# Optimization experiments

Measured on AMD Instinct MI355X. Metric: run time of the kernel, lower is better.

## Reference

```python
import jax, jax.numpy as jnp
import numpy as np

NUM_HEADS = 16


def setup_inputs() -> dict:
    key = jax.random.key(0)
    k1, k2, k3, k4 = jax.random.split(key, 4)
    in_dim, out_dim = 1024, 1024
    x = jax.random.normal(k1, (4, 2048, in_dim), dtype=jnp.float32)
    # nn.Linear weights stored as [out, in]; we keep that convention.
    s = 1.0 / np.sqrt(in_dim)
    Wq = jax.random.uniform(k2, (out_dim, in_dim), jnp.float32, -s, s)
    Wk = jax.random.uniform(k3, (out_dim, in_dim), jnp.float32, -s, s)
    Wv = jax.random.uniform(k4, (out_dim, in_dim), jnp.float32, -s, s)
    return {"x": x, "Wq": Wq, "Wk": Wk, "Wv": Wv}


def reference(x, Wq, Wk, Wv):
    b, n, _ = x.shape
    out_dim = Wq.shape[0]
    h = NUM_HEADS
    d = out_dim // h  # head_dim

    def split_heads(t):  # [b,n,out] -> [b,h,n,d]
        return t.reshape(b, n, h, d).transpose(0, 2, 1, 3)

    q = split_heads(x @ Wq.T)
    k = split_heads(x @ Wk.T)
    v = split_heads(x @ Wv.T)

    scores = jnp.einsum("bhqd,bhkd->bhqk", q, k) / jnp.sqrt(jnp.float32(d))
    causal = jnp.tril(jnp.ones((n, n), dtype=bool))
    scores = jnp.where(causal, scores, -jnp.inf)
    attn = jax.nn.softmax(scores, axis=-1)
    out = jnp.einsum("bhqk,bhkd->bhqd", attn, v)
    return out.transpose(0, 2, 1, 3).reshape(b, n, out_dim)
```

## Files before the change

### kernel.cpp

```cpp
#include <hip/hip_runtime.h>

typedef __attribute__((ext_vector_type(8))) short short8;
typedef __attribute__((ext_vector_type(4))) short short4v;
typedef __attribute__((ext_vector_type(4))) float floatx4;
typedef __attribute__((ext_vector_type(16))) float floatx16;
typedef __attribute__((ext_vector_type(2))) int iv2;

#define GLOBAL_AS __attribute__((address_space(1)))
#define LDS_AS __attribute__((address_space(3)))

__device__ __forceinline__ short f2bs(float f) {
    union { float f; unsigned u; } v; v.f = f;
    unsigned r = v.u + 0x7fffu + ((v.u >> 16) & 1u);
    return (short)(r >> 16);
}

#if __has_builtin(__builtin_amdgcn_cvt_pk_bf16_f32)
typedef __attribute__((ext_vector_type(2))) __bf16 bf16x2;
__device__ __forceinline__ unsigned pk2(float a, float b) {
    union { bf16x2 v; unsigned u; } u;
    u.v = __builtin_amdgcn_cvt_pk_bf16_f32(a, b);
    return u.u;
}
#else
__device__ __forceinline__ unsigned pk2(float a, float b) {
    union { float f; unsigned u; } x, y; x.f = a; y.f = b;
    return ((y.u + 0x8000u) & 0xffff0000u) | ((x.u + 0x8000u) >> 16);
}
#endif

__global__ __launch_bounds__(256) void cast_all(const float* __restrict__ x,
                                                const float* __restrict__ Wq,
                                                const float* __restrict__ Wk,
                                                const float* __restrict__ Wv,
                                                short* __restrict__ xb,
                                                short* __restrict__ wb) {
    int b = blockIdx.x;
    int t = threadIdx.x;
    const float* src;
    short* dst;
    int idx;
    if (b < 8192) {
        src = x; dst = xb; idx = b * 1024 + t * 4;
    } else {
        int r = b - 8192;
        int wz = r >> 10;
        src = (wz == 0) ? Wq : (wz == 1) ? Wk : Wv;
        dst = wb + wz * (1 << 20);
        idx = (r & 1023) * 1024 + t * 4;
    }
    float4 v = *(const float4*)(src + idx);
    short4v o;
    o.x = f2bs(v.x); o.y = f2bs(v.y); o.z = f2bs(v.z); o.w = f2bs(v.w);
    *(short4v*)(dst + idx) = o;
}

__global__ __launch_bounds__(256) void qkv_gemm(const short* __restrict__ xb,
                                                const short* __restrict__ wb,
                                                short* __restrict__ qout,
                                                short* __restrict__ kout,
                                                short* __restrict__ vtout) {
    __shared__ short As[2][128 * 64];
    __shared__ short Bs[2][128 * 64];
    const int K = 1024;
    int tid = threadIdx.x;
    int lane = tid & 63;
    int wid = tid >> 6;
    int quad = lane >> 4;
    int l16 = lane & 15;
    int wm = (wid >> 1) * 64;
    int wn = (wid & 1) * 64;
    int bx = blockIdx.x;
    int bm = ((bx >> 3) + ((bx & 7) << 3)) * 128;
    int bn = blockIdx.y * 128;
    const short* W = wb + (size_t)blockIdx.z * K * 1024;

    floatx4 acc[4][4];
#pragma unroll
    for (int i = 0; i < 4; i++)
#pragma unroll
        for (int j = 0; j < 4; j++) acc[i][j] = (floatx4){0.f, 0.f, 0.f, 0.f};

    int srow = tid >> 3;
    int ssw = ((tid & 7) ^ (srow & 7)) * 8;

#define STAGE_AB(cb, kk) do { \
    _Pragma("unroll") for (int l = 0; l < 4; l++) { \
        const short* g = xb + (size_t)(bm + srow + l * 32) * K + (kk) + ssw; \
        __builtin_amdgcn_global_load_lds((const GLOBAL_AS void*)g, \
            (LDS_AS void*)(&As[cb][0] + tid * 8 + l * 2048), 16, 0, 0); \
    } \
    _Pragma("unroll") for (int l = 0; l < 4; l++) { \
        const short* g = W + (size_t)(bn + srow + l * 32) * K + (kk) + ssw; \
        __builtin_amdgcn_global_load_lds((const GLOBAL_AS void*)g, \
            (LDS_AS void*)(&Bs[cb][0] + tid * 8 + l * 2048), 16, 0, 0); \
    } \
} while (0)

    STAGE_AB(0, 0);

    for (int T = 0; T < 16; T++) {
        int cur = T & 1;
        __builtin_amdgcn_sched_barrier(0);
        __builtin_amdgcn_s_barrier();
        __builtin_amdgcn_sched_barrier(0);
        if (T < 15) {
            STAGE_AB(cur ^ 1, (T + 1) * 64);
            asm volatile("s_waitcnt vmcnt(8)" ::: "memory");
        } else {
            asm volatile("s_waitcnt vmcnt(0)" ::: "memory");
        }
        __builtin_amdgcn_sched_barrier(0);
        __builtin_amdgcn_s_barrier();
        __builtin_amdgcn_sched_barrier(0);

        const short* Ac = &As[cur][0];
        const short* Bc = &Bs[cur][0];
#pragma unroll
        for (int s = 0; s < 2; s++) {
            int slot = ((s * 4 + quad) ^ (l16 & 7)) * 8;
            short8 af[4], bf[4];
#pragma unroll
            for (int i = 0; i < 4; i++)
                af[i] = *(const short8*)(Ac + (wm + i * 16 + l16) * 64 + slot);
#pragma unroll
            for (int j = 0; j < 4; j++)
                bf[j] = *(const short8*)(Bc + (wn + j * 16 + l16) * 64 + slot);
#pragma unroll
            for (int i = 0; i < 4; i++)
#pragma unroll
                for (int j = 0; j < 4; j++)
                    acc[i][j] = __builtin_amdgcn_mfma_f32_16x16x32_bf16(af[i], bf[j], acc[i][j], 0, 0, 0);
        }
    }
#undef STAGE_AB

    if (blockIdx.z == 2) {
#pragma unroll
        for (int i = 0; i < 4; i++) {
#pragma unroll
            for (int j = 0; j < 4; j++) {
                int m = bm + wm + i * 16 + quad * 4;
                int c = bn + wn + j * 16 + l16;
                int b = m >> 11, nn = m & 2047, h = c >> 6, dd = c & 63;
                short4v pk;
                pk.x = f2bs(acc[i][j][0]);
                pk.y = f2bs(acc[i][j][1]);
                pk.z = f2bs(acc[i][j][2]);
                pk.w = f2bs(acc[i][j][3]);
                *(short4v*)(vtout + ((size_t)(b * 16 + h) * 64 + dd) * 2048 + nn) = pk;
            }
        }
    } else {
        short* dst = (blockIdx.z == 0) ? qout : kout;
        float qs = (blockIdx.z == 0) ? 0.180336881f : 1.0f;
#pragma unroll
        for (int i = 0; i < 4; i++) {
#pragma unroll
            for (int j = 0; j < 4; j++) {
#pragma unroll
                for (int r = 0; r < 4; r++) {
                    int m = bm + wm + i * 16 + quad * 4 + r;
                    int c = bn + wn + j * 16 + l16;
                    dst[((size_t)((m >> 11) * 16 + (c >> 6)) * 2048 + (m & 2047)) * 64 + (c & 63)] =
                        f2bs(acc[i][j][r] * qs);
                }
            }
        }
    }
}

__global__ __launch_bounds__(256, 2) void attn(const short* __restrict__ q,
                                               const short* __restrict__ k,
                                               const short* __restrict__ vt,
                                               float* __restrict__ out) {
    __shared__ short Ks[2][128 * 64];
    __shared__ short Vs[2][64 * 128];

    int tid = threadIdx.x;
    int lane = tid & 63;
    int wid = tid >> 6;
    int l32 = lane & 31;
    int half = lane >> 5;

    int flat = blockIdx.x;
    int xcd = flat & 7;
    int slot = flat >> 3;
    int bh = xcd * 8 + (slot >> 3);
    int qx = slot & 7;
    int b = bh >> 4, h = bh & 15;

    const short* qp = q + (size_t)(b * 16 + h) * 2048 * 64;
    const short* kp = k + (size_t)(b * 16 + h) * 2048 * 64;
    const short* vp = vt + (size_t)(b * 16 + h) * 64 * 2048;

    int krow = tid >> 3;
    int ksw = ((tid & 7) ^ (krow & 7)) * 8;
    int vd = tid >> 4;
    int vc = tid & 15;
    int vsw = ((vc & 8) | ((vc ^ vd) & 7)) * 8;

#define BARRIER() asm volatile("s_barrier" ::: "memory")
#define STAGE_KV(cb, kvb) do { \
    _Pragma("unroll") for (int l = 0; l < 4; l++) { \
        const short* g = kp + (size_t)((kvb) + krow + l * 32) * 64 + ksw; \
        __builtin_amdgcn_global_load_lds((const GLOBAL_AS void*)g, \
            (LDS_AS void*)(&Ks[cb][0] + tid * 8 + l * 2048), 16, 0, 0); \
    } \
    _Pragma("unroll") for (int l = 0; l < 4; l++) { \
        const short* g = vp + (size_t)(vd + l * 16) * 2048 + (kvb) + vsw; \
        __builtin_amdgcn_global_load_lds((const GLOBAL_AS void*)g, \
            (LDS_AS void*)(&Vs[cb][0] + tid * 8 + l * 2048), 16, 0, 0); \
    } \
} while (0)

    for (int phase = 0; phase < 2; phase++) {
        int qt = (phase == 0) ? qx : (15 - qx);
        int qbase = qt * 128;
        int qrow_w = qbase + wid * 32;
        int qlane = qrow_w + l32;

        short8 qf[4];
#pragma unroll
        for (int s = 0; s < 4; s++)
            qf[s] = *(const short8*)(qp + (size_t)qlane * 64 + s * 16 + half * 8);

        floatx16 oacc[2];
#pragma unroll
        for (int nt = 0; nt < 2; nt++)
#pragma unroll
            for (int e = 0; e < 16; e++) oacc[nt][e] = 0.f;
        float rs = 0.f;

        int ntiles = qt + 1;

        BARRIER();
        STAGE_KV(0, 0);

        for (int t = 0; t < ntiles; t++) {
            int cur = t & 1;
            int kvb = t * 128;

            BARRIER();
            if (t + 1 < ntiles) {
                STAGE_KV(cur ^ 1, kvb + 128);
                asm volatile("s_waitcnt vmcnt(8)" ::: "memory");
            } else {
                asm volatile("s_waitcnt vmcnt(0)" ::: "memory");
            }
            BARRIER();

            const short* Kc = &Ks[cur][0];
            const short* Vc = &Vs[cur][0];

            floatx16 sacc[4];
#pragma unroll
            for (int kb = 0; kb < 4; kb++)
#pragma unroll
                for (int e = 0; e < 16; e++) sacc[kb][e] = 0.f;
            __builtin_amdgcn_s_setprio(1);
#pragma unroll
            for (int s = 0; s < 4; s++) {
#pragma unroll
                for (int kb = 0; kb < 4; kb++) {
                    int key = kb * 32 + l32;
                    int c = s * 2 + half;
                    short8 kf = *(const short8*)(Kc + key * 64 + ((c ^ (key & 7)) * 8));
                    sacc[kb] = __builtin_amdgcn_mfma_f32_32x32x16_bf16(kf, qf[s], sacc[kb], 0, 0, 0);
                }
            }
            __builtin_amdgcn_s_setprio(0);

            bool diag = (t == ntiles - 1) && (kvb + 127 > qrow_w);
            unsigned W0[4][4], W1[4][4];
#pragma unroll
            for (int kb = 0; kb < 4; kb++) {
#pragma unroll
                for (int e = 0; e < 16; e++) {
                    float p = __builtin_amdgcn_exp2f(sacc[kb][e]);
                    if (diag) {
                        int key = kvb + kb * 32 + (e & 3) + 8 * (e >> 2) + 4 * half;
                        p = (key > qlane) ? 0.f : p;
                    }
                    sacc[kb][e] = p;
                    rs += p;
                }
#pragma unroll
                for (int g = 0; g < 4; g++) {
                    W0[kb][g] = pk2(sacc[kb][4 * g + 0], sacc[kb][4 * g + 1]);
                    W1[kb][g] = pk2(sacc[kb][4 * g + 2], sacc[kb][4 * g + 3]);
                }
            }

            __builtin_amdgcn_s_setprio(1);
#pragma unroll
            for (int s = 0; s < 8; s++) {
                int kb = s >> 1;
                int g0 = (s & 1) * 2;
                int g1 = g0 + 1;
                iv2 r0 = __builtin_amdgcn_permlane32_swap(W0[kb][g0], W0[kb][g1], false, false);
                iv2 r1 = __builtin_amdgcn_permlane32_swap(W1[kb][g0], W1[kb][g1], false, false);
                union { int4 v; short8 s8; } pu;
                pu.v.x = r0.x; pu.v.y = r1.x; pu.v.z = r0.y; pu.v.w = r1.y;
                short8 pf = pu.s8;
#pragma unroll
                for (int nt = 0; nt < 2; nt++) {
                    int d = nt * 32 + l32;
                    int c = s * 2 + half;
                    int sl = (c & 8) | ((c ^ (d & 7)) & 7);
                    short8 vf = *(const short8*)(Vc + d * 128 + sl * 8);
                    oacc[nt] = __builtin_amdgcn_mfma_f32_32x32x16_bf16(pf, vf, oacc[nt], 0, 0, 0);
                }
            }
            __builtin_amdgcn_s_setprio(0);
        }

        float tot = rs + __shfl_xor(rs, 32);
        float inv = 1.0f / tot;
        float invr[16];
#pragma unroll
        for (int e = 0; e < 16; e++)
            invr[e] = __shfl(inv, (e & 3) + 8 * (e >> 2) + 4 * half);
#pragma unroll
        for (int nt = 0; nt < 2; nt++) {
#pragma unroll
            for (int e = 0; e < 16; e++) {
                int r = (e & 3) + 8 * (e >> 2) + 4 * half;
                int nn = qrow_w + r;
                out[((size_t)b * 2048 + nn) * 1024 + h * 64 + nt * 32 + l32] = oacc[nt][e] * invr[e];
            }
        }
    }
#undef STAGE_KV
#undef BARRIER
}

extern "C" void kernel_launch(void* const* d_in, const int* in_sizes, int n_in,
                              void* d_out, int out_size, void* d_ws, size_t ws_size,
                              hipStream_t stream) {
    const float* x = (const float*)d_in[0];
    const float* Wq = (const float*)d_in[1];
    const float* Wk = (const float*)d_in[2];
    const float* Wv = (const float*)d_in[3];
    float* out = (float*)d_out;
    char* ws = (char*)d_ws;

    short* xb = (short*)ws;
    short* wb = (short*)(ws + (16u << 20));
    short* qb = (short*)(ws + (22u << 20));
    short* kb = (short*)(ws + (38u << 20));
    short* vtb = (short*)(ws + (54u << 20));

    cast_all<<<8192 + 3 * 1024, 256, 0, stream>>>(x, Wq, Wk, Wv, xb, wb);
    qkv_gemm<<<dim3(64, 8, 3), 256, 0, stream>>>(xb, wb, qb, kb, vtb);
    attn<<<512, 256, 0, stream>>>(qb, kb, vtb, out);
}
```

Before: 198.2 us.

## Share streamed KV tiles between paired causal query tiles in one pass

```diff
diff --git a/kernel.cpp b/kernel.cpp
--- a/kernel.cpp
+++ b/kernel.cpp
@@ -70,8 +70,7 @@
     int l16 = lane & 15;
     int wm = (wid >> 1) * 64;
     int wn = (wid & 1) * 64;
-    int bx = blockIdx.x;
-    int bm = ((bx >> 3) + ((bx & 7) << 3)) * 128;
+    int bm = blockIdx.x * 128;
     int bn = blockIdx.y * 128;
     const short* W = wb + (size_t)blockIdx.z * K * 1024;
 
@@ -214,123 +213,128 @@
     } \
 } while (0)
 
-    for (int phase = 0; phase < 2; phase++) {
-        int qt = (phase == 0) ? qx : (15 - qx);
-        int qbase = qt * 128;
-        int qrow_w = qbase + wid * 32;
-        int qlane = qrow_w + l32;
-
-        short8 qf[4];
-#pragma unroll
-        for (int s = 0; s < 4; s++)
-            qf[s] = *(const short8*)(qp + (size_t)qlane * 64 + s * 16 + half * 8);
-
-        floatx16 oacc[2];
-#pragma unroll
-        for (int nt = 0; nt < 2; nt++)
-#pragma unroll
-            for (int e = 0; e < 16; e++) oacc[nt][e] = 0.f;
-        float rs = 0.f;
-
-        int ntiles = qt + 1;
+#define STREAM_TILE(qf, qlane, oacc, rs, isdiag) do { \
+    floatx16 sacc[4]; \
+    _Pragma("unroll") for (int kb = 0; kb < 4; kb++) \
+    _Pragma("unroll") for (int e = 0; e < 16; e++) sacc[kb][e] = 0.f; \
+    __builtin_amdgcn_s_setprio(1); \
+    _Pragma("unroll") for (int s = 0; s < 4; s++) { \
+        _Pragma("unroll") for (int kb = 0; kb < 4; kb++) { \
+            int key = kb * 32 + l32; \
+            int c = s * 2 + half; \
+            short8 kf = *(const short8*)(Kc + key * 64 + ((c ^ (key & 7)) * 8)); \
+            sacc[kb] = __builtin_amdgcn_mfma_f32_32x32x16_bf16(kf, qf[s], sacc[kb], 0, 0, 0); \
+        } \
+    } \
+    __builtin_amdgcn_s_setprio(0); \
+    unsigned W0[4][4], W1[4][4]; \
+    _Pragma("unroll") for (int kb = 0; kb < 4; kb++) { \
+        _Pragma("unroll") for (int e = 0; e < 16; e++) { \
+            float p = __builtin_amdgcn_exp2f(sacc[kb][e]); \
+            if (isdiag) { \
+                int key = kvb + kb * 32 + (e & 3) + 8 * (e >> 2) + 4 * half; \
+                p = (key > (qlane)) ? 0.f : p; \
+            } \
+            sacc[kb][e] = p; \
+            rs += p; \
+        } \
+        _Pragma("unroll") for (int g = 0; g < 4; g++) { \
+            W0[kb][g] = pk2(sacc[kb][4 * g + 0], sacc[kb][4 * g + 1]); \
+            W1[kb][g] = pk2(sacc[kb][4 * g + 2], sacc[kb][4 * g + 3]); \
+        } \
+    } \
+    __builtin_amdgcn_s_setprio(1); \
+    _Pragma("unroll") for (int s = 0; s < 8; s++) { \
+        int kb = s >> 1; \
+        int g0 = (s & 1) * 2; \
+        int g1 = g0 + 1; \
+        iv2 r0 = __builtin_amdgcn_permlane32_swap(W0[kb][g0], W0[kb][g1], false, false); \
+        iv2 r1 = __builtin_amdgcn_permlane32_swap(W1[kb][g0], W1[kb][g1], false, false); \
+        union { int4 v; short8 s8; } pu; \
+        pu.v.x = r0.x; pu.v.y = r1.x; pu.v.z = r0.y; pu.v.w = r1.y; \
+        short8 pf = pu.s8; \
+        _Pragma("unroll") for (int nt = 0; nt < 2; nt++) { \
+            int d = nt * 32 + l32; \
+            int c = s * 2 + half; \
+            int sl = (c & 8) | ((c ^ (d & 7)) & 7); \
+            short8 vf = *(const short8*)(Vc + d * 128 + sl * 8); \
+            oacc[nt] = __builtin_amdgcn_mfma_f32_32x32x16_bf16(pf, vf, oacc[nt], 0, 0, 0); \
+        } \
+    } \
+    __builtin_amdgcn_s_setprio(0); \
+} while (0)
+
+#define EPILOG(rs, oacc, qrow_w) do { \
+    float tot = (rs) + __shfl_xor((rs), 32); \
+    float inv = 1.0f / tot; \
+    float invr[16]; \
+    _Pragma("unroll") for (int e = 0; e < 16; e++) \
+        invr[e] = __shfl(inv, (e & 3) + 8 * (e >> 2) + 4 * half); \
+    _Pragma("unroll") for (int nt = 0; nt < 2; nt++) { \
+        _Pragma("unroll") for (int e = 0; e < 16; e++) { \
+            int r = (e & 3) + 8 * (e >> 2) + 4 * half; \
+            int nn = (qrow_w) + r; \
+            out[((size_t)b * 2048 + nn) * 1024 + h * 64 + nt * 32 + l32] = oacc[nt][e] * invr[e]; \
+        } \
+    } \
+} while (0)
+
+    int qA = qx;
+    int qB = 15 - qx;
+    int NT = qB + 1;
+
+    int qrowA = qA * 128 + wid * 32;
+    int qrowB = qB * 128 + wid * 32;
+    int qlaneA = qrowA + l32;
+    int qlaneB = qrowB + l32;
+
+    short8 qfA[4], qfB[4];
+#pragma unroll
+    for (int s = 0; s < 4; s++) {
+        qfA[s] = *(const short8*)(qp + (size_t)qlaneA * 64 + s * 16 + half * 8);
+        qfB[s] = *(const short8*)(qp + (size_t)qlaneB * 64 + s * 16 + half * 8);
+    }
+
+    floatx16 oaccA[2], oaccB[2];
+#pragma unroll
+    for (int nt = 0; nt < 2; nt++)
+#pragma unroll
+        for (int e = 0; e < 16; e++) { oaccA[nt][e] = 0.f; oaccB[nt][e] = 0.f; }
+    float rsA = 0.f, rsB = 0.f;
+
+    STAGE_KV(0, 0);
+
+    for (int t = 0; t < NT; t++) {
+        int cur = t & 1;
+        int kvb = t * 128;
 
         BARRIER();
-        STAGE_KV(0, 0);
-
-        for (int t = 0; t < ntiles; t++) {
-            int cur = t & 1;
-            int kvb = t * 128;
-
-            BARRIER();
-            if (t + 1 < ntiles) {
-                STAGE_KV(cur ^ 1, kvb + 128);
-                asm volatile("s_waitcnt vmcnt(8)" ::: "memory");
-            } else {
-                asm volatile("s_waitcnt vmcnt(0)" ::: "memory");
-            }
-            BARRIER();
-
-            const short* Kc = &Ks[cur][0];
-            const short* Vc = &Vs[cur][0];
-
-            floatx16 sacc[4];
-#pragma unroll
-            for (int kb = 0; kb < 4; kb++)
-#pragma unroll
-                for (int e = 0; e < 16; e++) sacc[kb][e] = 0.f;
-            __builtin_amdgcn_s_setprio(1);
-#pragma unroll
-            for (int s = 0; s < 4; s++) {
-#pragma unroll
-                for (int kb = 0; kb < 4; kb++) {
-                    int key = kb * 32 + l32;
-                    int c = s * 2 + half;
-                    short8 kf = *(const short8*)(Kc + key * 64 + ((c ^ (key & 7)) * 8));
-                    sacc[kb] = __builtin_amdgcn_mfma_f32_32x32x16_bf16(kf, qf[s], sacc[kb], 0, 0, 0);
-                }
-            }
-            __builtin_amdgcn_s_setprio(0);
-
-            bool diag = (t == ntiles - 1) && (kvb + 127 > qrow_w);
-            unsigned W0[4][4], W1[4][4];
-#pragma unroll
-            for (int kb = 0; kb < 4; kb++) {
-#pragma unroll
-                for (int e = 0; e < 16; e++) {
-                    float p = __builtin_amdgcn_exp2f(sacc[kb][e]);
-                    if (diag) {
-                        int key = kvb + kb * 32 + (e & 3) + 8 * (e >> 2) + 4 * half;
-                        p = (key > qlane) ? 0.f : p;
-                    }
-                    sacc[kb][e] = p;
-                    rs += p;
-                }
-#pragma unroll
-                for (int g = 0; g < 4; g++) {
-                    W0[kb][g] = pk2(sacc[kb][4 * g + 0], sacc[kb][4 * g + 1]);
-                    W1[kb][g] = pk2(sacc[kb][4 * g + 2], sacc[kb][4 * g + 3]);
-                }
-            }
-
-            __builtin_amdgcn_s_setprio(1);
-#pragma unroll
-            for (int s = 0; s < 8; s++) {
-                int kb = s >> 1;
-                int g0 = (s & 1) * 2;
-                int g1 = g0 + 1;
-                iv2 r0 = __builtin_amdgcn_permlane32_swap(W0[kb][g0], W0[kb][g1], false, false);
-                iv2 r1 = __builtin_amdgcn_permlane32_swap(W1[kb][g0], W1[kb][g1], false, false);
-                union { int4 v; short8 s8; } pu;
-                pu.v.x = r0.x; pu.v.y = r1.x; pu.v.z = r0.y; pu.v.w = r1.y;
-                short8 pf = pu.s8;
-#pragma unroll
-                for (int nt = 0; nt < 2; nt++) {
-                    int d = nt * 32 + l32;
-                    int c = s * 2 + half;
-                    int sl = (c & 8) | ((c ^ (d & 7)) & 7);
-                    short8 vf = *(const short8*)(Vc + d * 128 + sl * 8);
-                    oacc[nt] = __builtin_amdgcn_mfma_f32_32x32x16_bf16(pf, vf, oacc[nt], 0, 0, 0);
-                }
-            }
-            __builtin_amdgcn_s_setprio(0);
-        }
-
-        float tot = rs + __shfl_xor(rs, 32);
-        float inv = 1.0f / tot;
-        float invr[16];
-#pragma unroll
-        for (int e = 0; e < 16; e++)
-            invr[e] = __shfl(inv, (e & 3) + 8 * (e >> 2) + 4 * half);
-#pragma unroll
-        for (int nt = 0; nt < 2; nt++) {
-#pragma unroll
-            for (int e = 0; e < 16; e++) {
-                int r = (e & 3) + 8 * (e >> 2) + 4 * half;
-                int nn = qrow_w + r;
-                out[((size_t)b * 2048 + nn) * 1024 + h * 64 + nt * 32 + l32] = oacc[nt][e] * invr[e];
-            }
-        }
-    }
+        if (t + 1 < NT) {
+            STAGE_KV(cur ^ 1, kvb + 128);
+            asm volatile("s_waitcnt vmcnt(8)" ::: "memory");
+        } else {
+            asm volatile("s_waitcnt vmcnt(0)" ::: "memory");
+        }
+        BARRIER();
+
+        const short* Kc = &Ks[cur][0];
+        const short* Vc = &Vs[cur][0];
+
+        if (t <= qA) {
+            bool dA = (t == qA);
+            STREAM_TILE(qfA, qlaneA, oaccA, rsA, dA);
+        }
+        {
+            bool dB = (t == NT - 1);
+            STREAM_TILE(qfB, qlaneB, oaccB, rsB, dB);
+        }
+    }
+
+    EPILOG(rsA, oaccA, qrowA);
+    EPILOG(rsB, oaccB, qrowB);
+
+#undef STREAM_TILE
+#undef EPILOG
 #undef STAGE_KV
 #undef BARRIER
 }
```

Result: slower. 209.4 us (median of 2 runs) (+5.6%).
